# Performance work log

Hardware: AMD Instinct MI355X
Metric: run time of the kernel (lower is better)

The kernel has to match this reference:

```python
import jax, jax.numpy as jnp
import numpy as np

B, C, M, K, V, D, H, A, L, HF = 2, 128, 4, 4, 64, 1024, 16, 64, 4, 2048
E = M + K
EPS = 1e-5
THETA = 10000.0


def _rmsnorm(x, w):
    return x * jax.lax.rsqrt(jnp.mean(x * x, -1, keepdims=True) + EPS) * w


def _l2norm(x):
    n = jnp.sqrt(jnp.sum(x * x, -1, keepdims=True))
    return x / jnp.maximum(n, EPS)


def _rope(x, cos, sin):
    x1, x2 = jnp.split(x, 2, axis=-1)
    return jnp.concatenate([x1 * cos + x2 * sin, -x1 * sin + x2 * cos], -1)


def _forward(x_input, dec_w1, dec_w2, pos_emb, Wqkv, Wo, Wup, Wdown, attn_norm_w, ffn_norm_w, doc):
    b = x_input.shape[0]
    c = x_input.shape[1] // M
    # decoder_w1 then 'b (c m) (k v) -> b c k (m v)', decoder_w2, pos emb
    x = jnp.einsum('bsd,od->bso', x_input, dec_w1)
    x = x.reshape(b, c, M, K, V).transpose(0, 1, 3, 2, 4).reshape(b, c, K, M * V)
    x = jnp.einsum('bcku,du->bckd', x, dec_w2) + pos_emb
    # decoder_include_original_token: prepend original m tokens per block
    x = jnp.concatenate([x_input.reshape(b, c, M, D), x], axis=2).reshape(b, c * E, D)
    s = c * E
    # mask_mod (decoder_global_original_attn): (causal & kv%e<k & same_doc) | same_block
    idx = jnp.arange(s)
    blk = idx // E
    docs = doc[:, blk]  # [b, s]
    doc_m = docs[:, :, None] == docs[:, None, :]
    causal = blk[:, None] >= blk[None, :]
    kv_ok = (idx % E) < K
    same = blk[:, None] == blk[None, :]
    mask = (causal[None] & kv_ok[None, None, :] & doc_m) | same[None]  # [b, s, s]
    # rotary tables (applied post head-split, dim A)
    inv_freq = (1.0 / THETA) ** (jnp.arange(0, A, 2) / A)
    freqs = jnp.arange(s)[:, None] * inv_freq[None, :]
    cos, sin = jnp.cos(freqs), jnp.sin(freqs)  # [s, A/2]
    scale = 1.0 / jnp.sqrt(jnp.float32(A))
    neg = jnp.float32(-1e30)

    def heads(t):
        return t.reshape(b, s, H, A).transpose(0, 2, 1, 3)

    for li in range(L):
        xn = _rmsnorm(x, attn_norm_w[li])
        qkv = jnp.einsum('bsd,od->bso', xn, Wqkv[li])
        q, k, v = jnp.split(qkv, 3, axis=-1)
        q, k, v = heads(q), heads(k), heads(v)
        q, k = _l2norm(q), _l2norm(k)  # qk_norm
        q, k = _rope(q, cos, sin), _rope(k, cos, sin)
        scores = jnp.einsum('bhqa,bhka->bhqk', q, k) * scale
        scores = jnp.where(mask[:, None], scores, neg)
        probs = jax.nn.softmax(scores, axis=-1)
        attn = jnp.einsum('bhqk,bhka->bhqa', probs, v)
        attn = attn.transpose(0, 2, 1, 3).reshape(b, s, D)
        x1_in = jnp.einsum('bsd,od->bso', attn, Wo[li]) + x
        xf = _rmsnorm(x1_in, ffn_norm_w[li])
        up = jnp.einsum('bsd,od->bso', xf, Wup[li])
        u1, u2 = jnp.split(up, 2, axis=-1)
        x = jnp.einsum('bsh,dh->bsd', jax.nn.silu(u1) * u2, Wdown[li]) + x1_in
    # 'b (c e) d -> (b c) e d' then drop original tokens
    return x.reshape(b * c, E, D)[:, M:]


def setup_inputs() -> dict:
    key = jax.random.key(0)
    ks = jax.random.split(key, 10)
    sc = 0.02
    return {
        'x_input': jax.random.normal(ks[0], (B, C * M, D), jnp.float32),
        'doc': jnp.sort(jax.random.randint(ks[1], (B, C), 0, 4), axis=-1),
        'dec_w1': jax.random.normal(ks[2], (K * V, D), jnp.float32) * sc,
        'dec_w2': jax.random.normal(ks[3], (D, M * V), jnp.float32) * sc,
        'pos_emb': jax.random.normal(ks[4], (1, 1, K, D), jnp.float32) * sc,
        'Wqkv': jax.random.normal(ks[5], (L, 3 * D, D), jnp.float32) * sc,
        'Wo': jax.random.normal(ks[6], (L, D, D), jnp.float32) * sc,
        'Wup': jax.random.normal(ks[7], (L, 2 * HF, D), jnp.float32) * sc,
        'Wdown': jax.random.normal(ks[8], (L, D, HF), jnp.float32) * sc,
        'attn_norm_w': jnp.ones((L, D), jnp.float32),
        'ffn_norm_w': jnp.ones((L, D), jnp.float32),
    }


def reference(x_input, doc, dec_w1, dec_w2, pos_emb, Wqkv, Wo, Wup, Wdown, attn_norm_w, ffn_norm_w):
    return _forward(x_input, dec_w1, dec_w2, pos_emb, Wqkv, Wo, Wup, Wdown, attn_norm_w, ffn_norm_w, doc)
```

## Files before the change

### kernel.cpp

```cpp
#include <hip/hip_runtime.h>
#include <hip/hip_bf16.h>

typedef __bf16 bf16;
typedef __bf16 bf16x8 __attribute__((ext_vector_type(8)));
typedef __bf16 bf16x4 __attribute__((ext_vector_type(4)));
typedef float  f32x4  __attribute__((ext_vector_type(4)));

#define MFMA16(a, b, c) __builtin_amdgcn_mfma_f32_16x16x32_bf16(a, b, c, 0, 0, 0)

template <int EPI, int AF32, int BF32, int TM, int TN, int SK = 1>
__global__ __launch_bounds__(256 * SK) void gemm_bt(
    const void* __restrict__ Av, const void* __restrict__ Bv,
    const float* __restrict__ Res, void* __restrict__ Out,
    int Ntot, int Ktot, int lda)
{
    constexpr int PA = TM / 64, PB = TN / 64;
    constexpr int WN = (TN == 128) ? ((TM == 128) ? 2 : 4) : 2;
    constexpr int WM = 4 / WN;
    constexpr int I = TM / (WM * 16), J = TN / (WN * 16);
    __shared__ __align__(16) bf16 As[2][SK][TM][40];
    __shared__ __align__(16) bf16 Bs[2][SK][TN][40];
    static_assert(SK == 1 || sizeof(As) >= TM * TN * 4, "combine buffer fits in As");
    const int tid  = threadIdx.x;
    const int grp  = (SK > 1) ? (tid >> 8) : 0;
    const int t8   = tid & 255;
    const int wave = t8 >> 6, lane = tid & 63;
    const int quad = lane >> 4, l16 = lane & 15;
    const int wm = wave / WN, wn = wave % WN;
    const int rowW = wm * (TM / WM), colW = wn * (TN / WN);
    const int rowBase = blockIdx.y * TM, colBase = blockIdx.x * TN;

    f32x4 acc[I][J];
    const f32x4 z4 = {0.f, 0.f, 0.f, 0.f};
#pragma unroll
    for (int i = 0; i < I; i++)
#pragma unroll
        for (int j = 0; j < J; j++) acc[i][j] = z4;

    float4 rAf[PA][2]; bf16x8 rAb[PA];
    float4 rBf[PB][2]; bf16x8 rBb[PB];

    auto loadTile = [&](int kt) {
#pragma unroll
        for (int p = 0; p < PA; p++) {
            int ch = p * 256 + t8, r = ch >> 2, c8 = (ch & 3) << 3;
            if (AF32) {
                const float* s = (const float*)Av + (size_t)(rowBase + r) * lda + kt + c8;
                rAf[p][0] = *(const float4*)s; rAf[p][1] = *(const float4*)(s + 4);
            } else {
                rAb[p] = *(const bf16x8*)((const bf16*)Av + (size_t)(rowBase + r) * lda + kt + c8);
            }
        }
#pragma unroll
        for (int p = 0; p < PB; p++) {
            int ch = p * 256 + t8, r = ch >> 2, c8 = (ch & 3) << 3;
            if (BF32) {
                const float* s = (const float*)Bv + (size_t)(colBase + r) * Ktot + kt + c8;
                rBf[p][0] = *(const float4*)s; rBf[p][1] = *(const float4*)(s + 4);
            } else {
                rBb[p] = *(const bf16x8*)((const bf16*)Bv + (size_t)(colBase + r) * Ktot + kt + c8);
            }
        }
    };
    auto storeTile = [&](int buf) {
#pragma unroll
        for (int p = 0; p < PA; p++) {
            int ch = p * 256 + t8, r = ch >> 2, c8 = (ch & 3) << 3;
            bf16x8 t;
            if (AF32) {
                t[0]=(bf16)rAf[p][0].x; t[1]=(bf16)rAf[p][0].y; t[2]=(bf16)rAf[p][0].z; t[3]=(bf16)rAf[p][0].w;
                t[4]=(bf16)rAf[p][1].x; t[5]=(bf16)rAf[p][1].y; t[6]=(bf16)rAf[p][1].z; t[7]=(bf16)rAf[p][1].w;
            } else t = rAb[p];
            *(bf16x8*)&As[buf][grp][r][c8] = t;
        }
#pragma unroll
        for (int p = 0; p < PB; p++) {
            int ch = p * 256 + t8, r = ch >> 2, c8 = (ch & 3) << 3;
            bf16x8 t;
            if (BF32) {
                t[0]=(bf16)rBf[p][0].x; t[1]=(bf16)rBf[p][0].y; t[2]=(bf16)rBf[p][0].z; t[3]=(bf16)rBf[p][0].w;
                t[4]=(bf16)rBf[p][1].x; t[5]=(bf16)rBf[p][1].y; t[6]=(bf16)rBf[p][1].z; t[7]=(bf16)rBf[p][1].w;
            } else t = rBb[p];
            *(bf16x8*)&Bs[buf][grp][r][c8] = t;
        }
    };

    const int Kgrp  = Ktot / SK;
    const int kbase = grp * Kgrp;
    loadTile(kbase);
    storeTile(0);
    __syncthreads();
    const int nk = Kgrp >> 5;
    for (int k = 0; k < nk; k++) {
        const bool more = (k + 1) < nk;
        if (more) loadTile(kbase + ((k + 1) << 5));
        const int buf = k & 1;
        bf16x8 af[I], bfr[J];
#pragma unroll
        for (int i = 0; i < I; i++)
            af[i] = *(const bf16x8*)&As[buf][grp][rowW + i * 16 + l16][quad * 8];
#pragma unroll
        for (int j = 0; j < J; j++)
            bfr[j] = *(const bf16x8*)&Bs[buf][grp][colW + j * 16 + l16][quad * 8];
#pragma unroll
        for (int i = 0; i < I; i++)
#pragma unroll
            for (int j = 0; j < J; j++)
                acc[i][j] = MFMA16(af[i], bfr[j], acc[i][j]);
        if (more) { storeTile(buf ^ 1); __syncthreads(); }
    }

    if (SK == 2) {
        __syncthreads();
        float* red = (float*)&As[0][0][0][0];
        if (grp == 1) {
#pragma unroll
            for (int i = 0; i < I; i++)
#pragma unroll
                for (int j = 0; j < J; j++)
#pragma unroll
                    for (int r = 0; r < 4; r++)
                        red[(rowW + i * 16 + quad * 4 + r) * TN +
                            (colW + j * 16 + l16)] = acc[i][j][r];
        }
        __syncthreads();
        if (grp != 0) return;
#pragma unroll
        for (int i = 0; i < I; i++)
#pragma unroll
            for (int j = 0; j < J; j++)
#pragma unroll
                for (int r = 0; r < 4; r++)
                    acc[i][j][r] += red[(rowW + i * 16 + quad * 4 + r) * TN +
                                        (colW + j * 16 + l16)];
    }

#pragma unroll
    for (int i = 0; i < I; i++) {
        int row0 = rowBase + rowW + i * 16 + quad * 4;
#pragma unroll
        for (int j = 0; j < J; j++) {
            int col = colBase + colW + j * 16 + l16;
#pragma unroll
            for (int r = 0; r < 4; r++) {
                size_t off = (size_t)(row0 + r) * Ntot + col;
                float v = acc[i][j][r];
                if (EPI == 0)      ((bf16*)Out)[off]  = (bf16)v;
                else if (EPI == 1) ((float*)Out)[off] = v + Res[off];
                else               ((float*)Out)[off] = v;
            }
        }
    }
}

__global__ __launch_bounds__(512) void gemm_up_swiglu(
    const bf16* __restrict__ A, const float* __restrict__ B,
    bf16* __restrict__ Out)
{
    __shared__ __align__(16) bf16 Smem[2][2][256][40];
    const int tid  = threadIdx.x;
    const int grp  = tid >> 8, t8 = tid & 255;
    const int wave = t8 >> 6, lane = tid & 63;
    const int quad = lane >> 4, l16 = lane & 15;
    const int wm = wave >> 1, wn = wave & 1;
    const int rowBase = blockIdx.y * 128, cb = blockIdx.x;

    f32x4 acc[4][4];
    const f32x4 z4 = {0.f, 0.f, 0.f, 0.f};
#pragma unroll
    for (int i = 0; i < 4; i++)
#pragma unroll
        for (int j = 0; j < 4; j++) acc[i][j] = z4;

    bf16x8 rA[2]; float4 rB[2][2];
    auto loadTile = [&](int kt) {
#pragma unroll
        for (int p = 0; p < 2; p++) {
            int ch = p * 256 + t8, r = ch >> 2, c8 = (ch & 3) << 3;
            rA[p] = *(const bf16x8*)(A + (size_t)(rowBase + r) * 1024 + kt + c8);
            int brow = (r >> 6) * 2048 + cb * 64 + (r & 63);
            const float* s = B + (size_t)brow * 1024 + kt + c8;
            rB[p][0] = *(const float4*)s; rB[p][1] = *(const float4*)(s + 4);
        }
    };
    auto storeTile = [&](int buf) {
#pragma unroll
        for (int p = 0; p < 2; p++) {
            int ch = p * 256 + t8, r = ch >> 2, c8 = (ch & 3) << 3;
            *(bf16x8*)&Smem[buf][grp][r][c8] = rA[p];
            bf16x8 t;
            t[0]=(bf16)rB[p][0].x; t[1]=(bf16)rB[p][0].y; t[2]=(bf16)rB[p][0].z; t[3]=(bf16)rB[p][0].w;
            t[4]=(bf16)rB[p][1].x; t[5]=(bf16)rB[p][1].y; t[6]=(bf16)rB[p][1].z; t[7]=(bf16)rB[p][1].w;
            *(bf16x8*)&Smem[buf][grp][128 + r][c8] = t;
        }
    };

    const int kbase = grp * 512;
    loadTile(kbase);
    storeTile(0);
    __syncthreads();
    for (int k = 0; k < 16; k++) {
        const bool more = k < 15;
        if (more) loadTile(kbase + ((k + 1) << 5));
        const int buf = k & 1;
        bf16x8 af[4], bfr[4];
#pragma unroll
        for (int i = 0; i < 4; i++)
            af[i] = *(const bf16x8*)&Smem[buf][grp][wm * 64 + i * 16 + l16][quad * 8];
#pragma unroll
        for (int j = 0; j < 4; j++) {
            int brow = (j < 2) ? (wn * 32 + j * 16) : (64 + wn * 32 + (j - 2) * 16);
            bfr[j] = *(const bf16x8*)&Smem[buf][grp][128 + brow + l16][quad * 8];
        }
#pragma unroll
        for (int i = 0; i < 4; i++)
#pragma unroll
            for (int j = 0; j < 4; j++)
                acc[i][j] = MFMA16(af[i], bfr[j], acc[i][j]);
        if (more) { storeTile(buf ^ 1); __syncthreads(); }
    }

    __syncthreads();
    float* red = (float*)&Smem[0][0][0][0];
    if (grp == 1) {
#pragma unroll
        for (int i = 0; i < 4; i++)
#pragma unroll
            for (int j = 0; j < 4; j++) {
                int brow = ((j < 2) ? (wn * 32 + j * 16)
                                    : (64 + wn * 32 + (j - 2) * 16)) + l16;
#pragma unroll
                for (int r = 0; r < 4; r++)
                    red[(wm * 64 + i * 16 + quad * 4 + r) * 128 + brow] = acc[i][j][r];
            }
    }
    __syncthreads();
    if (grp != 0) return;
#pragma unroll
    for (int i = 0; i < 4; i++)
#pragma unroll
        for (int j = 0; j < 4; j++) {
            int brow = ((j < 2) ? (wn * 32 + j * 16)
                                : (64 + wn * 32 + (j - 2) * 16)) + l16;
#pragma unroll
            for (int r = 0; r < 4; r++)
                acc[i][j][r] += red[(wm * 64 + i * 16 + quad * 4 + r) * 128 + brow];
        }

#pragma unroll
    for (int i = 0; i < 4; i++) {
        int row0 = rowBase + wm * 64 + i * 16 + quad * 4;
#pragma unroll
        for (int jj = 0; jj < 2; jj++) {
            int col = cb * 64 + wn * 32 + jj * 16 + l16;
#pragma unroll
            for (int r = 0; r < 4; r++) {
                float u1 = acc[i][jj][r], u2 = acc[i][jj + 2][r];
                float g = u1 / (1.f + __expf(-u1));
                Out[(size_t)(row0 + r) * 2048 + col] = (bf16)(g * u2);
            }
        }
    }
}

__global__ __launch_bounds__(256) void rmsnorm_k(
    const float* __restrict__ X, const float* __restrict__ W,
    bf16* __restrict__ Out)
{
    const int row = blockIdx.x, tid = threadIdx.x;
    const float4 xv = *(const float4*)(X + (size_t)row * 1024 + tid * 4);
    float ss = xv.x * xv.x + xv.y * xv.y + xv.z * xv.z + xv.w * xv.w;
#pragma unroll
    for (int m = 1; m < 64; m <<= 1) ss += __shfl_xor(ss, m);
    __shared__ float red[4];
    if ((tid & 63) == 0) red[tid >> 6] = ss;
    __syncthreads();
    float tot = red[0] + red[1] + red[2] + red[3];
    float sc = rsqrtf(tot * (1.0f / 1024.0f) + 1e-5f);
    const float4 wv = *(const float4*)(W + tid * 4);
    bf16x4 o;
    o[0] = (bf16)(xv.x * sc * wv.x);
    o[1] = (bf16)(xv.y * sc * wv.y);
    o[2] = (bf16)(xv.z * sc * wv.z);
    o[3] = (bf16)(xv.w * sc * wv.w);
    *(bf16x4*)(Out + (size_t)row * 1024 + tid * 4) = o;
}

__global__ __launch_bounds__(256) void ropetab_k(float* __restrict__ tab)
{
    int i = blockIdx.x * 256 + threadIdx.x;
    int s = i >> 5, j = i & 31;
    float f = (float)s * __expf(-(float)j * 0.2878231366242557f);
    tab[i * 2]     = cosf(f);
    tab[i * 2 + 1] = sinf(f);
}

__global__ __launch_bounds__(256) void qkprep_k(
    bf16* __restrict__ qkv, const float* __restrict__ tab)
{
    int wid  = blockIdx.x * 4 + (threadIdx.x >> 6);
    int lane = threadIdx.x & 63;
    int s = wid & 1023, h = (wid >> 10) & 15, b = (wid >> 14) & 1, op = wid >> 15;
    bf16* addr = qkv + ((size_t)(b * 1024 + s)) * 3072 + op * 1024 + h * 64 + lane;
    float v = (float)*addr;
    float ss = v * v;
#pragma unroll
    for (int m = 1; m < 64; m <<= 1) ss += __shfl_xor(ss, m);
    v /= fmaxf(sqrtf(ss), 1e-5f);
    float2 cssn = ((const float2*)tab)[(s << 5) + (lane & 31)];
    float partner = __shfl_xor(v, 32);
    float o = (lane < 32) ? (v * cssn.x + partner * cssn.y)
                          : (v * cssn.x - partner * cssn.y);
    if (op == 0) o *= 0.125f;
    *addr = (bf16)o;
}

__global__ __launch_bounds__(256) void vtrans_k(
    const bf16* __restrict__ qkv, bf16* __restrict__ Vt)
{
    __shared__ __align__(16) bf16 Ls[64][72];
    const int st = blockIdx.x, h = blockIdx.y, b = blockIdx.z;
    const int tid = threadIdx.x;
#pragma unroll
    for (int p = 0; p < 2; p++) {
        int s = p * 32 + (tid >> 3), a0 = (tid & 7) << 3;
        *(bf16x8*)&Ls[s][a0] = *(const bf16x8*)(
            qkv + ((size_t)(b * 1024 + st * 64 + s)) * 3072 + 2048 + h * 64 + a0);
    }
    __syncthreads();
#pragma unroll
    for (int p = 0; p < 2; p++) {
        int a = p * 32 + (tid >> 3), s0 = (tid & 7) << 3;
        bf16x8 v;
#pragma unroll
        for (int j = 0; j < 8; j++) v[j] = Ls[s0 + j][a];
        *(bf16x8*)(Vt + (((size_t)((b * 16 + h) * 64 + a)) << 10) + st * 64 + s0) = v;
    }
}

__global__ __launch_bounds__(512) void attn_k(
    const bf16* __restrict__ qkv, const bf16* __restrict__ Vt,
    const int* __restrict__ doc, bf16* __restrict__ attnb)
{
    const int p = blockIdx.x, h = blockIdx.y, b = blockIdx.z;
    const int tid = threadIdx.x, w8 = tid >> 6, lane = tid & 63;
    const int w = w8 & 3, half = w8 >> 2;
    const int quad = lane >> 4, l16 = lane & 15;
    __shared__ __align__(16) bf16 PsT[8][64][20];
    __shared__ float cmb[4][64][20];
    __shared__ int docL[128];
    if (tid < 128) docL[tid] = doc[b * 128 + tid];
    __syncthreads();

    const int g = (w == 0) ? p : (w == 1) ? 31 - p : (w == 2) ? 32 + p : 63 - p;
    const bf16* qp = qkv + ((size_t)(b * 1024 + g * 16 + l16)) * 3072 + h * 64 + quad * 8;
    const bf16x8 qf0 = *(const bf16x8*)qp;
    const bf16x8 qf1 = *(const bf16x8*)(qp + 32);
    const bf16* Kbase = qkv + ((size_t)(b * 1024)) * 3072 + 1024 + h * 64;
    const bf16* Vbase = Vt + (((size_t)((b * 16 + h) * 64)) << 10);

    const f32x4 z4 = {0.f, 0.f, 0.f, 0.f};
    f32x4 O[4] = {z4, z4, z4, z4};
    float lp[4] = {0.f, 0.f, 0.f, 0.f};

    int bq[4], dq[4];
#pragma unroll
    for (int r = 0; r < 4; r++) {
        bq[r] = (g * 16 + quad * 4 + r) >> 3;
        dq[r] = docL[bq[r]];
    }

    bf16x8 kc[8], kn[8];
    auto loadK = [&](int kt, bf16x8* dst) {
        const bf16* kp = Kbase + (size_t)(kt * 64 + l16) * 3072 + quad * 8;
#pragma unroll
        for (int kg = 0; kg < 4; kg++) {
            dst[kg * 2]     = *(const bf16x8*)(kp + (size_t)kg * 16 * 3072);
            dst[kg * 2 + 1] = *(const bf16x8*)(kp + (size_t)kg * 16 * 3072 + 32);
        }
    };

    const int T   = (g + 4) >> 2;
    const int Th  = (T + 1) >> 1;
    const int kt0 = half ? Th : 0;
    const int kt1 = half ? T  : Th;

    if (kt0 < kt1) {
        loadK(kt0, kc);
        for (int kt = kt0; kt < kt1; kt++) {
            const int k0 = kt * 64;
            f32x4 sf[4];
#pragma unroll
            for (int kg = 0; kg < 4; kg++) {
                sf[kg] = z4;
                sf[kg] = MFMA16(qf0, kc[kg * 2],     sf[kg]);
                sf[kg] = MFMA16(qf1, kc[kg * 2 + 1], sf[kg]);
            }
            bf16x8 vr[4][2];
#pragma unroll
            for (int t = 0; t < 4; t++)
#pragma unroll
                for (int c = 0; c < 2; c++)
                    vr[t][c] = *(const bf16x8*)(
                        Vbase + ((size_t)(t * 16 + l16) << 10) + k0 + c * 32 + quad * 8);
            if (kt + 1 < kt1) loadK(kt + 1, kn);

            float pvv[4][4];
#pragma unroll
            for (int kg = 0; kg < 4; kg++) {
                int kgi = k0 + kg * 16 + l16;
                int bk  = kgi >> 3;
                int dkv = docL[bk];
                bool kbit = (kgi & 7) < 4;
#pragma unroll
                for (int r = 0; r < 4; r++) {
                    bool ok = (bq[r] == bk) || ((bq[r] >= bk) && kbit && (dq[r] == dkv));
                    float pp = ok ? __expf(sf[kg][r]) : 0.f;
                    pvv[kg][r] = pp;
                    lp[r] += pp;
                }
            }
#pragma unroll
            for (int kg = 0; kg < 4; kg++) {
                bf16x4 t4;
#pragma unroll
                for (int r = 0; r < 4; r++) t4[r] = (bf16)pvv[kg][r];
                *(bf16x4*)&PsT[w8][kg * 16 + l16][quad * 4] = t4;
            }
            bf16x8 pa0, pa1;
#pragma unroll
            for (int j = 0; j < 8; j++) {
                pa0[j] = PsT[w8][quad * 8 + j][l16];
                pa1[j] = PsT[w8][32 + quad * 8 + j][l16];
            }
#pragma unroll
            for (int t = 0; t < 4; t++) {
                O[t] = MFMA16(pa0, vr[t][0], O[t]);
                O[t] = MFMA16(pa1, vr[t][1], O[t]);
            }
            if (kt + 1 < kt1) {
#pragma unroll
                for (int i = 0; i < 8; i++) kc[i] = kn[i];
            }
        }
    }

    if (half) {
#pragma unroll
        for (int t = 0; t < 4; t++)
#pragma unroll
            for (int r = 0; r < 4; r++) cmb[w][lane][t * 4 + r] = O[t][r];
#pragma unroll
        for (int r = 0; r < 4; r++) cmb[w][lane][16 + r] = lp[r];
    }
    __syncthreads();
    if (half) return;
#pragma unroll
    for (int t = 0; t < 4; t++)
#pragma unroll
        for (int r = 0; r < 4; r++) O[t][r] += cmb[w][lane][t * 4 + r];
#pragma unroll
    for (int r = 0; r < 4; r++) lp[r] += cmb[w][lane][16 + r];

#pragma unroll
    for (int r = 0; r < 4; r++) {
#pragma unroll
        for (int m = 1; m < 16; m <<= 1) lp[r] += __shfl_xor(lp[r], m);
    }

#pragma unroll
    for (int t = 0; t < 4; t++)
#pragma unroll
        for (int r = 0; r < 4; r++) {
            int qg = g * 16 + quad * 4 + r;
            float v = O[t][r] / fmaxf(lp[r], 1e-20f);
            attnb[((size_t)(b * 1024) + qg) * 1024 + h * 64 + t * 16 + l16] = (bf16)v;
        }
}

__global__ __launch_bounds__(256) void permute_k(
    const bf16* __restrict__ t1, bf16* __restrict__ t1p)
{
    int idx = blockIdx.x * 256 + threadIdx.x;
    int u = idx & 255, m = u >> 6, v = u & 63;
    int orow = idx >> 8;
    int k = orow & 3, bc = orow >> 2;
    int b = bc >> 7, c = bc & 127;
    t1p[idx] = t1[((size_t)(b * 512 + c * 4 + m)) * 256 + k * 64 + v];
}

__global__ __launch_bounds__(256) void buildx_k(
    const float* __restrict__ x_input, const float* __restrict__ t2,
    const float* __restrict__ pos_emb, float* __restrict__ xres)
{
    int idx = blockIdx.x * 256 + threadIdx.x;
    int d = idx & 1023, row = idx >> 10;
    int b = row >> 10, rr = row & 1023;
    int c = rr >> 3, e = rr & 7;
    float v;
    if (e < 4)
        v = x_input[((size_t)(b * 512 + c * 4 + e)) * 1024 + d];
    else
        v = t2[((size_t)(b * 512 + c * 4 + (e - 4))) * 1024 + d] +
            pos_emb[(e - 4) * 1024 + d];
    xres[idx] = v;
}

__global__ __launch_bounds__(256) void finalout_k(
    const float* __restrict__ xres, float* __restrict__ out)
{
    int idx = blockIdx.x * 256 + threadIdx.x;
    int d = idx & 1023, t = idx >> 10;
    int kk = t & 3, bc = t >> 2;
    int b = bc >> 7, c = bc & 127;
    out[idx] = xres[((size_t)(b * 1024 + c * 8 + 4 + kk)) * 1024 + d];
}

extern "C" void kernel_launch(void* const* d_in, const int* in_sizes, int n_in,
                              void* d_out, int out_size, void* d_ws, size_t ws_size,
                              hipStream_t stream)
{
    const float* x_input = (const float*)d_in[0];
    const int*   doc     = (const int*)d_in[1];
    const float* dec_w1  = (const float*)d_in[2];
    const float* dec_w2  = (const float*)d_in[3];
    const float* pos_emb = (const float*)d_in[4];
    const float* Wqkv    = (const float*)d_in[5];
    const float* Wo      = (const float*)d_in[6];
    const float* Wup     = (const float*)d_in[7];
    const float* Wdown   = (const float*)d_in[8];
    const float* anw     = (const float*)d_in[9];
    const float* fnw     = (const float*)d_in[10];
    float* out = (float*)d_out;

    char* w = (char*)d_ws;
    float* xres  = (float*)(w);
    bf16*  attnb = (bf16*)(w + (8u << 20));
    bf16*  t1    = (bf16*)(w + (8u << 20));
    bf16*  t1p   = (bf16*)(w + (8u << 20) + (512u << 10));
    bf16*  Vt    = (bf16*)(w + (12u << 20));
    bf16*  xn2   = (bf16*)(w + (12u << 20));
    bf16*  qkv   = (bf16*)(w + (16u << 20));
    float* t2    = (float*)(w + (16u << 20));
    float* x1res = (float*)(w + (16u << 20));
    bf16*  hg    = (bf16*)(w + (24u << 20));
    bf16*  xn1   = (bf16*)(w + (28u << 20));
    float* rtab  = out;

    ropetab_k<<<128, 256, 0, stream>>>(rtab);
    gemm_bt<0, 1, 1, 64, 64><<<dim3(4, 16), 256, 0, stream>>>(
        x_input, dec_w1, nullptr, t1, 256, 1024, 1024);
    permute_k<<<1024, 256, 0, stream>>>(t1, t1p);
    gemm_bt<2, 0, 1, 64, 64><<<dim3(16, 16), 256, 0, stream>>>(
        t1p, dec_w2, nullptr, t2, 1024, 256, 256);
    buildx_k<<<8192, 256, 0, stream>>>(x_input, t2, pos_emb, xres);

    for (int li = 0; li < 4; ++li) {
        rmsnorm_k<<<2048, 256, 0, stream>>>(xres, anw + li * 1024, xn1);
        gemm_bt<0, 0, 1, 128, 128><<<dim3(24, 16), 256, 0, stream>>>(
            xn1, Wqkv + (size_t)li * 3072 * 1024, nullptr, qkv, 3072, 1024, 1024);
        qkprep_k<<<16384, 256, 0, stream>>>(qkv, rtab);
        vtrans_k<<<dim3(16, 16, 2), 256, 0, stream>>>(qkv, Vt);
        attn_k<<<dim3(16, 16, 2), 512, 0, stream>>>(qkv, Vt, doc, attnb);
        gemm_bt<1, 0, 1, 64, 64, 2><<<dim3(16, 32), 512, 0, stream>>>(
            attnb, Wo + (size_t)li * 1024 * 1024, xres, x1res, 1024, 1024, 1024);
        rmsnorm_k<<<2048, 256, 0, stream>>>(x1res, fnw + li * 1024, xn2);
        gemm_up_swiglu<<<dim3(32, 16), 512, 0, stream>>>(
            xn2, Wup + (size_t)li * 4096 * 1024, hg);
        gemm_bt<1, 0, 1, 64, 64, 2><<<dim3(16, 32), 512, 0, stream>>>(
            hg, Wdown + (size_t)li * 1024 * 2048, x1res, xres, 1024, 2048, 2048);
    }

    finalout_k<<<4096, 256, 0, stream>>>(xres, out);
}
```

Before: 902.1 us.

## Share K/V tiles across waves via double-buffered LDS in attention kernel

```diff
diff --git a/kernel.cpp b/kernel.cpp
--- a/kernel.cpp
+++ b/kernel.cpp
@@ -338,21 +338,23 @@
     }
 }
 
-__global__ __launch_bounds__(512) void attn_k(
+__global__ __launch_bounds__(256) void attn_k(
     const bf16* __restrict__ qkv, const bf16* __restrict__ Vt,
     const int* __restrict__ doc, bf16* __restrict__ attnb)
 {
     const int p = blockIdx.x, h = blockIdx.y, b = blockIdx.z;
-    const int tid = threadIdx.x, w8 = tid >> 6, lane = tid & 63;
-    const int w = w8 & 3, half = w8 >> 2;
+    const int tid = threadIdx.x, w = tid >> 6, lane = tid & 63;
     const int quad = lane >> 4, l16 = lane & 15;
-    __shared__ __align__(16) bf16 PsT[8][64][20];
-    __shared__ float cmb[4][64][20];
+    __shared__ __align__(16) bf16 Ks[2][64][72];
+    __shared__ __align__(16) bf16 Vs[2][64][72];
+    __shared__ __align__(16) bf16 PsT[4][64][20];
     __shared__ int docL[128];
     if (tid < 128) docL[tid] = doc[b * 128 + tid];
-    __syncthreads();
-
-    const int g = (w == 0) ? p : (w == 1) ? 31 - p : (w == 2) ? 32 + p : 63 - p;
+
+    const int g = 4 * p + w;
+    const int Tw   = (g + 4) >> 2;
+    const int maxT = (4 * p + 7) >> 2;
+
     const bf16* qp = qkv + ((size_t)(b * 1024 + g * 16 + l16)) * 3072 + h * 64 + quad * 8;
     const bf16x8 qf0 = *(const bf16x8*)qp;
     const bf16x8 qf1 = *(const bf16x8*)(qp + 32);
@@ -363,6 +365,7 @@
     f32x4 O[4] = {z4, z4, z4, z4};
     float lp[4] = {0.f, 0.f, 0.f, 0.f};
 
+    __syncthreads();
     int bq[4], dq[4];
 #pragma unroll
     for (int r = 0; r < 4; r++) {
@@ -370,41 +373,42 @@
         dq[r] = docL[bq[r]];
     }
 
-    bf16x8 kc[8], kn[8];
-    auto loadK = [&](int kt, bf16x8* dst) {
-        const bf16* kp = Kbase + (size_t)(kt * 64 + l16) * 3072 + quad * 8;
-#pragma unroll
-        for (int kg = 0; kg < 4; kg++) {
-            dst[kg * 2]     = *(const bf16x8*)(kp + (size_t)kg * 16 * 3072);
-            dst[kg * 2 + 1] = *(const bf16x8*)(kp + (size_t)kg * 16 * 3072 + 32);
+    bf16x8 rK[2], rV[2];
+    auto stageRegs = [&](int kt) {
+#pragma unroll
+        for (int c = 0; c < 2; c++) {
+            int ch = c * 256 + tid, r = ch >> 3, c8 = (ch & 7) << 3;
+            rK[c] = *(const bf16x8*)(Kbase + (size_t)(kt * 64 + r) * 3072 + c8);
+            rV[c] = *(const bf16x8*)(Vbase + ((size_t)r << 10) + kt * 64 + c8);
         }
     };
-
-    const int T   = (g + 4) >> 2;
-    const int Th  = (T + 1) >> 1;
-    const int kt0 = half ? Th : 0;
-    const int kt1 = half ? T  : Th;
-
-    if (kt0 < kt1) {
-        loadK(kt0, kc);
-        for (int kt = kt0; kt < kt1; kt++) {
+    auto stageLDS = [&](int buf) {
+#pragma unroll
+        for (int c = 0; c < 2; c++) {
+            int ch = c * 256 + tid, r = ch >> 3, c8 = (ch & 7) << 3;
+            *(bf16x8*)&Ks[buf][r][c8] = rK[c];
+            *(bf16x8*)&Vs[buf][r][c8] = rV[c];
+        }
+    };
+
+    stageRegs(0);
+    stageLDS(0);
+    __syncthreads();
+    for (int kt = 0; kt < maxT; kt++) {
+        const bool more = (kt + 1) < maxT;
+        if (more) stageRegs(kt + 1);
+        const int buf = kt & 1;
+        if (kt < Tw) {
             const int k0 = kt * 64;
             f32x4 sf[4];
 #pragma unroll
             for (int kg = 0; kg < 4; kg++) {
+                const bf16x8 k0f = *(const bf16x8*)&Ks[buf][kg * 16 + l16][quad * 8];
+                const bf16x8 k1f = *(const bf16x8*)&Ks[buf][kg * 16 + l16][32 + quad * 8];
                 sf[kg] = z4;
-                sf[kg] = MFMA16(qf0, kc[kg * 2],     sf[kg]);
-                sf[kg] = MFMA16(qf1, kc[kg * 2 + 1], sf[kg]);
-            }
-            bf16x8 vr[4][2];
-#pragma unroll
-            for (int t = 0; t < 4; t++)
-#pragma unroll
-                for (int c = 0; c < 2; c++)
-                    vr[t][c] = *(const bf16x8*)(
-                        Vbase + ((size_t)(t * 16 + l16) << 10) + k0 + c * 32 + quad * 8);
-            if (kt + 1 < kt1) loadK(kt + 1, kn);
-
+                sf[kg] = MFMA16(qf0, k0f, sf[kg]);
+                sf[kg] = MFMA16(qf1, k1f, sf[kg]);
+            }
             float pvv[4][4];
 #pragma unroll
             for (int kg = 0; kg < 4; kg++) {
@@ -425,42 +429,25 @@
                 bf16x4 t4;
 #pragma unroll
                 for (int r = 0; r < 4; r++) t4[r] = (bf16)pvv[kg][r];
-                *(bf16x4*)&PsT[w8][kg * 16 + l16][quad * 4] = t4;
+                *(bf16x4*)&PsT[w][kg * 16 + l16][quad * 4] = t4;
             }
             bf16x8 pa0, pa1;
 #pragma unroll
             for (int j = 0; j < 8; j++) {
-                pa0[j] = PsT[w8][quad * 8 + j][l16];
-                pa1[j] = PsT[w8][32 + quad * 8 + j][l16];
+                pa0[j] = PsT[w][quad * 8 + j][l16];
+                pa1[j] = PsT[w][32 + quad * 8 + j][l16];
             }
 #pragma unroll
             for (int t = 0; t < 4; t++) {
-                O[t] = MFMA16(pa0, vr[t][0], O[t]);
-                O[t] = MFMA16(pa1, vr[t][1], O[t]);
-            }
-            if (kt + 1 < kt1) {
-#pragma unroll
-                for (int i = 0; i < 8; i++) kc[i] = kn[i];
-            }
-        }
-    }
-
-    if (half) {
-#pragma unroll
-        for (int t = 0; t < 4; t++)
-#pragma unroll
-            for (int r = 0; r < 4; r++) cmb[w][lane][t * 4 + r] = O[t][r];
-#pragma unroll
-        for (int r = 0; r < 4; r++) cmb[w][lane][16 + r] = lp[r];
-    }
-    __syncthreads();
-    if (half) return;
-#pragma unroll
-    for (int t = 0; t < 4; t++)
-#pragma unroll
-        for (int r = 0; r < 4; r++) O[t][r] += cmb[w][lane][t * 4 + r];
-#pragma unroll
-    for (int r = 0; r < 4; r++) lp[r] += cmb[w][lane][16 + r];
+                const bf16x8 v0f = *(const bf16x8*)&Vs[buf][t * 16 + l16][quad * 8];
+                const bf16x8 v1f = *(const bf16x8*)&Vs[buf][t * 16 + l16][32 + quad * 8];
+                O[t] = MFMA16(pa0, v0f, O[t]);
+                O[t] = MFMA16(pa1, v1f, O[t]);
+            }
+        }
+        if (more) stageLDS(buf ^ 1);
+        __syncthreads();
+    }
 
 #pragma unroll
     for (int r = 0; r < 4; r++) {
@@ -561,7 +548,7 @@
             xn1, Wqkv + (size_t)li * 3072 * 1024, nullptr, qkv, 3072, 1024, 1024);
         qkprep_k<<<16384, 256, 0, stream>>>(qkv, rtab);
         vtrans_k<<<dim3(16, 16, 2), 256, 0, stream>>>(qkv, Vt);
-        attn_k<<<dim3(16, 16, 2), 512, 0, stream>>>(qkv, Vt, doc, attnb);
+        attn_k<<<dim3(16, 16, 2), 256, 0, stream>>>(qkv, Vt, doc, attnb);
         gemm_bt<1, 0, 1, 64, 64, 2><<<dim3(16, 32), 512, 0, stream>>>(
             attnb, Wo + (size_t)li * 1024 * 1024, xres, x1res, 1024, 1024, 1024);
         rmsnorm_k<<<2048, 256, 0, stream>>>(x1res, fnw + li * 1024, xn2);
```

Result: no change. 885.5 us (-1.8%).
